# Optimization experiments

Hardware: AMD Instinct MI355X
Metric: run time of the kernel (lower is better)

Reference implementation:

```python
import jax, jax.numpy as jnp
import numpy as np
import math

INPUT_DIM = 1024
QUERY_DIM = 1024
VALUE_DIM = 1024

def setup_inputs() -> dict:
    key = jax.random.key(0)
    ks = jax.random.split(key, 7)
    N, T, D = 4, 4096, INPUT_DIM
    s_in = 1.0 / math.sqrt(D)
    X = jax.random.normal(ks[0], (N, T, D), dtype=jnp.float32)
    # torch.nn.Linear weights: (out, in), init ~ U(-1/sqrt(in), 1/sqrt(in))
    Wq = jax.random.uniform(ks[1], (QUERY_DIM, D), jnp.float32, -s_in, s_in)
    bq = jax.random.uniform(ks[2], (QUERY_DIM,), jnp.float32, -s_in, s_in)
    Wk = jax.random.uniform(ks[3], (QUERY_DIM, D), jnp.float32, -s_in, s_in)
    bk = jax.random.uniform(ks[4], (QUERY_DIM,), jnp.float32, -s_in, s_in)
    Wv = jax.random.uniform(ks[5], (VALUE_DIM, D), jnp.float32, -s_in, s_in)
    bv = jax.random.uniform(ks[6], (VALUE_DIM,), jnp.float32, -s_in, s_in)
    return {"X": X, "Wq": Wq, "bq": bq, "Wk": Wk, "bk": bk, "Wv": Wv, "bv": bv}

def reference(X, Wq, bq, Wk, bk, Wv, bv):
    N, T, D = X.shape
    q = jnp.einsum('ntd,qd->ntq', X, Wq) + bq  # (N,T,Q)
    k = jnp.einsum('ntd,qd->ntq', X, Wk) + bk  # (N,T,Q)
    v = jnp.einsum('ntd,vd->ntv', X, Wv) + bv  # (N,T,V)
    # NOTE: original scales by sqrt(D) = sqrt(input_dim), not sqrt(query_dim)
    scores = jnp.einsum('ntq,nsq->nts', q, k) / jnp.sqrt(jnp.asarray(D, X.dtype))
    attn = jax.nn.softmax(scores, axis=-1)  # (N,T,T)
    return jnp.einsum('nts,nsv->ntv', attn, v)
```

## Files before the change

kernel.cpp:

```cpp
#include <hip/hip_runtime.h>
#include <stdint.h>

typedef unsigned short u16;
typedef unsigned char u8;
typedef unsigned int u32;
typedef short shortx8 __attribute__((ext_vector_type(8)));
typedef float floatx4 __attribute__((ext_vector_type(4)));
typedef int intx4 __attribute__((ext_vector_type(4)));
typedef int intx8 __attribute__((ext_vector_type(8)));

__device__ __forceinline__ u16 f2bf(float f) {
    u32 u = __builtin_bit_cast(u32, f);
    u = (u + 0x7fffu + ((u >> 16) & 1u)) >> 16;
    return (u16)u;
}

#if defined(__has_builtin)
#  if __has_builtin(__builtin_amdgcn_cvt_pk_fp8_f32)
#    define HAVE_CVT_FP8 1
#  endif
#  if __has_builtin(__builtin_amdgcn_global_load_lds)
#    define HAVE_GLL 1
#  endif
#endif
#ifndef HAVE_CVT_FP8
#  define HAVE_CVT_FP8 0
#endif
#ifndef HAVE_GLL
#  define HAVE_GLL 0
#endif

__device__ __forceinline__ u8 f2fp8(float f) {
#if HAVE_CVT_FP8
    return (u8)(__builtin_amdgcn_cvt_pk_fp8_f32(f, f, 0, false) & 0xff);
#else
    u32 u = __builtin_bit_cast(u32, f);
    u32 s = (u >> 24) & 0x80u;
    u32 m = u & 0x7fffffffu;
    if (m >= 0x43e00000u) return (u8)(s | 0x7eu);
    if (m < 0x3c800000u) {
        int q = __float2int_rn(__builtin_bit_cast(float, m) * 512.f);
        return (u8)(s | (u32)q);
    }
    u32 r = m + 0x7ffffu + ((m >> 20) & 1u);
    u32 code = (((r >> 23) - 120u) << 3) | ((r >> 20) & 7u);
    if (code > 0x7eu) code = 0x7eu;
    return (u8)(s | code);
#endif
}

#if HAVE_GLL
__device__ __forceinline__ void gload_lds16(const void* g, void* l) {
    __builtin_amdgcn_global_load_lds(
        (const __attribute__((address_space(1))) u32*)g,
        (__attribute__((address_space(3))) u32*)l,
        16, 0, 0);
}
#endif

template <typename OutT, int MODE, int SWZ>
__global__ __launch_bounds__(256, 2) void gemm_bt(
    const u16* __restrict__ Ag, const u16* __restrict__ Bg, OutT* __restrict__ Cg,
    int lda, int ldb, int ldc, int K,
    const float* __restrict__ aux, float scale,
    long long sAz, long long sBz, long long sCz, long long sXz,
    int swz_nhalf)
{
    __shared__ u16 smem[4][128 * 32];

    int z, mb, nb;
    if constexpr (SWZ) {
        const int f = blockIdx.x, xcd = f & 7, g = f >> 3;
        z = xcd >> 1;
        mb = g & 31;
        nb = (xcd & 1) * swz_nhalf + (g >> 5);
    } else {
        z = blockIdx.z; mb = blockIdx.y; nb = blockIdx.x;
    }
    const int m0 = mb * 128, n0 = nb * 128;

    const u16* A = Ag + (long long)z * sAz;
    const u16* B = Bg + (long long)z * sBz;
    OutT* C = Cg + (long long)z * sCz;
    const float* auxp = aux ? aux + (long long)z * sXz : nullptr;

    const int tid = threadIdx.x, lane = tid & 63, wv = tid >> 6;

    const int srow = lane >> 2;
    const int schunk = (lane & 3) * 8;
    const u16* gA0 = A + (size_t)(m0 + wv * 16 + srow) * lda + schunk;
    const u16* gA1 = gA0 + (size_t)64 * lda;
    const u16* gB0 = B + (size_t)(n0 + wv * 16 + srow) * ldb + schunk;
    const u16* gB1 = gB0 + (size_t)64 * ldb;
    const int wb = wv * 512;

    const int wm = (wv & 1) * 64, wn = (wv >> 1) * 64;
    const int mi = lane & 15, kq = lane >> 4;

    floatx4 acc[4][4] = {};

    for (int k0 = 0; k0 < K; k0 += 64) {
#if HAVE_GLL
        gload_lds16(gA0,      &smem[0][wb]);
        gload_lds16(gA1,      &smem[0][2048 + wb]);
        gload_lds16(gA0 + 32, &smem[1][wb]);
        gload_lds16(gA1 + 32, &smem[1][2048 + wb]);
        gload_lds16(gB0,      &smem[2][wb]);
        gload_lds16(gB1,      &smem[2][2048 + wb]);
        gload_lds16(gB0 + 32, &smem[3][wb]);
        gload_lds16(gB1 + 32, &smem[3][2048 + wb]);
#else
        *(shortx8*)(&smem[0][wb] + lane * 8)        = *(const shortx8*)gA0;
        *(shortx8*)(&smem[0][2048 + wb] + lane * 8) = *(const shortx8*)gA1;
        *(shortx8*)(&smem[1][wb] + lane * 8)        = *(const shortx8*)(gA0 + 32);
        *(shortx8*)(&smem[1][2048 + wb] + lane * 8) = *(const shortx8*)(gA1 + 32);
        *(shortx8*)(&smem[2][wb] + lane * 8)        = *(const shortx8*)gB0;
        *(shortx8*)(&smem[2][2048 + wb] + lane * 8) = *(const shortx8*)gB1;
        *(shortx8*)(&smem[3][wb] + lane * 8)        = *(const shortx8*)(gB0 + 32);
        *(shortx8*)(&smem[3][2048 + wb] + lane * 8) = *(const shortx8*)(gB1 + 32);
#endif
        gA0 += 64; gA1 += 64; gB0 += 64; gB1 += 64;
        __syncthreads();

#pragma unroll
        for (int h = 0; h < 2; h++) {
            const u16* Ap = smem[h];
            const u16* Bp = smem[2 + h];
            shortx8 af[4], bfr[4];
#pragma unroll
            for (int i = 0; i < 4; i++)
                af[i] = *(const shortx8*)(Ap + (wm + i * 16 + mi) * 32 + kq * 8);
#pragma unroll
            for (int j = 0; j < 4; j++)
                bfr[j] = *(const shortx8*)(Bp + (wn + j * 16 + mi) * 32 + kq * 8);
#pragma unroll
            for (int i = 0; i < 4; i++)
#pragma unroll
                for (int j = 0; j < 4; j++)
                    acc[i][j] = __builtin_amdgcn_mfma_f32_16x16x32_bf16(
                        af[i], bfr[j], acc[i][j], 0, 0, 0);
        }
        __syncthreads();
    }

    float cb[4];
    if constexpr (MODE == 1) {
#pragma unroll
        for (int j = 0; j < 4; j++) cb[j] = auxp[n0 + wn + j * 16 + mi];
    }

    if constexpr (sizeof(OutT) == 2) {
        u16* ct = &smem[0][0];
#pragma unroll
        for (int i = 0; i < 4; i++) {
#pragma unroll
            for (int r = 0; r < 4; r++) {
                const int lrow = wm + i * 16 + kq * 4 + r;
                float radd = 0.f;
                if constexpr (MODE == 2) radd = auxp[m0 + lrow];
#pragma unroll
                for (int j = 0; j < 4; j++) {
                    float v = acc[i][j][r];
                    if constexpr (MODE == 1) v += cb[j];
                    if constexpr (MODE == 2) v += radd;
                    ct[lrow * 128 + wn + j * 16 + mi] = f2bf(v);
                }
            }
        }
        __syncthreads();
#pragma unroll
        for (int it = 0; it < 8; it++) {
            const int fl = (it * 256 + tid) * 8;
            const int row = fl >> 7, col = fl & 127;
            *(uint4*)(C + (size_t)(m0 + row) * ldc + n0 + col) =
                *(const uint4*)(ct + fl);
        }
    } else if constexpr (sizeof(OutT) == 1) {
        u8* ct = (u8*)&smem[0][0];
#pragma unroll
        for (int i = 0; i < 4; i++) {
#pragma unroll
            for (int r = 0; r < 4; r++) {
                const int lrow = wm + i * 16 + kq * 4 + r;
#pragma unroll
                for (int j = 0; j < 4; j++) {
                    float v = acc[i][j][r];
                    if constexpr (MODE == 1) v += cb[j];
                    ct[lrow * 128 + wn + j * 16 + mi] = f2fp8(v);
                }
            }
        }
        __syncthreads();
        u8* base = (u8*)Cg + ((size_t)mb * 16 + nb) * 16384;
#pragma unroll
        for (int it = 0; it < 4; it++) {
            const int fl = (it * 256 + tid) * 16;
            const int row = fl >> 7, c = (fl >> 4) & 7;
            *(uint4*)(base + row * 128 + ((c ^ (row & 7)) << 4)) =
                *(const uint4*)(ct + fl);
        }
    } else {
#pragma unroll
        for (int i = 0; i < 4; i++) {
#pragma unroll
            for (int r = 0; r < 4; r++) {
                const int row = m0 + wm + i * 16 + kq * 4 + r;
                float rmul = 1.f;
                if constexpr (MODE == 4) rmul = 1.0f / auxp[row];
                OutT* crow = C + (size_t)row * ldc;
#pragma unroll
                for (int j = 0; j < 4; j++) {
                    const int col = n0 + wn + j * 16 + mi;
                    crow[col] = acc[i][j][r] * rmul;
                }
            }
        }
    }
}

__global__ __launch_bounds__(512, 2) void gemm_pv256(
    const u16* __restrict__ Pg, const u16* __restrict__ Vt,
    float* __restrict__ outg, const float* __restrict__ sums, int T, int NT)
{
    __shared__ u8 smem[2][65536];

    const int f = blockIdx.x, xcd = f & 7, g = f >> 3;
    const int z = xcd >> 1;
    const int nb = (xcd & 1) * 2 + (g >> 4);
    const int mb = g & 15;
    const int m0 = mb * 256, n0 = nb * 256;

    const u8* Pz = (const u8*)(Pg + (size_t)z * T * T);
    const u8* Vz = (const u8*)(Vt + (size_t)z * T);
    const float* sumz = sums + (size_t)z * T;

    const int tid = threadIdx.x, lane = tid & 63, wv = tid >> 6;
    const int wr = wv >> 2, wc = wv & 3;
    const int mi = lane & 15, kq = lane >> 4;

    const int srow = lane >> 3;
    const int schunk = ((lane & 7) ^ srow) << 4;
    const size_t ldPb = (size_t)T * 2, ldVb = (size_t)NT * 2;
    const u8* gsrc;
    size_t grstride;
    int lds_r0;
    if (wv < 4) {
        gsrc = Pz + (size_t)(m0 + wv * 64 + srow) * ldPb + schunk;
        grstride = ldPb * 8;
        lds_r0 = wv * 8192;
    } else {
        gsrc = Vz + (size_t)(n0 + (wv - 4) * 64 + srow) * ldVb + schunk;
        grstride = ldVb * 8;
        lds_r0 = 32768 + (wv - 4) * 8192;
    }

    const int csw0 = ((0 * 4 + kq) ^ (mi & 7)) << 4;
    const int csw1 = ((1 * 4 + kq) ^ (mi & 7)) << 4;

    floatx4 acc[8][4] = {};

    auto stage = [&](int slot, int kt) {
        const u8* s0 = gsrc + (size_t)kt * 128;
        u8* l0 = &smem[slot][lds_r0];
#if HAVE_GLL
#pragma unroll
        for (int q = 0; q < 8; q++)
            gload_lds16(s0 + (size_t)q * grstride, l0 + q * 1024);
#else
#pragma unroll
        for (int q = 0; q < 8; q++)
            *(uint4*)(l0 + q * 1024 + lane * 16) =
                *(const uint4*)(s0 + (size_t)q * grstride);
#endif
    };

    stage(0, 0);
    __syncthreads();

    for (int kt = 0; kt < 64; kt++) {
        const int s = kt & 1;
        if (kt < 63) stage(s ^ 1, kt + 1);
        __builtin_amdgcn_sched_barrier(0);

        const u8* Ab = &smem[s][0];
        const u8* Bb = &smem[s][32768];

        shortx8 bfr[4][2];
#pragma unroll
        for (int nj = 0; nj < 4; nj++) {
            const u8* p = Bb + (wc * 64 + nj * 16 + mi) * 128;
            bfr[nj][0] = *(const shortx8*)(p + csw0);
            bfr[nj][1] = *(const shortx8*)(p + csw1);
        }
#pragma unroll
        for (int mh = 0; mh < 2; mh++) {
            shortx8 af[4][2];
#pragma unroll
            for (int fi = 0; fi < 4; fi++) {
                const u8* p = Ab + (wr * 128 + (mh * 4 + fi) * 16 + mi) * 128;
                af[fi][0] = *(const shortx8*)(p + csw0);
                af[fi][1] = *(const shortx8*)(p + csw1);
            }
            __builtin_amdgcn_s_setprio(1);
#pragma unroll
            for (int ks = 0; ks < 2; ks++)
#pragma unroll
                for (int fi = 0; fi < 4; fi++)
#pragma unroll
                    for (int nj = 0; nj < 4; nj++)
                        acc[mh * 4 + fi][nj] = __builtin_amdgcn_mfma_f32_16x16x32_bf16(
                            af[fi][ks], bfr[nj][ks], acc[mh * 4 + fi][nj], 0, 0, 0);
            __builtin_amdgcn_s_setprio(0);
        }
        __syncthreads();
    }

#pragma unroll
    for (int fr = 0; fr < 8; fr++) {
#pragma unroll
        for (int r = 0; r < 4; r++) {
            const int row = m0 + wr * 128 + fr * 16 + kq * 4 + r;
            const float rmul = 1.0f / sumz[row];
            float* crow = outg + ((size_t)z * T + row) * 1024 + n0 + wc * 64 + mi;
#pragma unroll
            for (int nj = 0; nj < 4; nj++)
                crow[nj * 16] = acc[fr][nj][r] * rmul;
        }
    }
}

__device__ __forceinline__ intx8 cat8(intx4 a, intx4 b) {
    return __builtin_shufflevector(a, b, 0, 1, 2, 3, 4, 5, 6, 7);
}

template <int SWZ>
__global__ __launch_bounds__(512, 2) void gemm_fp8_scores(
    const u8* __restrict__ QKt, u16* __restrict__ Pg,
    float* __restrict__ sums, float scale, int T)
{
    __shared__ u8 smem[2][32768];

    int z, mb, nb;
    if constexpr (SWZ) {
        const int f = blockIdx.x, xcd = f & 7, g = f >> 3;
        z = xcd >> 1;
        const int s = g >> 7, t = g & 127;
        mb = (s << 3) | (t & 7);
        nb = (xcd & 1) * 16 + (t >> 3);
    } else {
        z = blockIdx.z; mb = blockIdx.y; nb = blockIdx.x;
    }
    const int m0 = mb * 128, n0 = nb * 128;

    const u8* At = QKt + ((size_t)(z * 32 + mb) * 16) * 16384;
    const u8* Bt = QKt + ((size_t)(z * 32 + nb) * 16 + 8) * 16384;
    u16* P = Pg + (size_t)z * T * T;
    float* sumz = sums + (size_t)z * T;

    const int tid = threadIdx.x, lane = tid & 63, wv = tid >> 6;
    const int wm = (wv >> 1) * 32, wn = (wv & 1) * 64;
    const int mi = lane & 15, kq = lane >> 4;
    const int xm = mi & 7;
    const int off0 = ((2 * kq) ^ xm) * 16;
    const int off1 = ((2 * kq + 1) ^ xm) * 16;

    const u8* gA = At + wv * 2048 + lane * 16;
    const u8* gB = Bt + wv * 2048 + lane * 16;

    floatx4 acc[2][4] = {};

    auto stageP = [&](int b) {
#if HAVE_GLL
        gload_lds16(gA,        &smem[b][wv * 2048]);
        gload_lds16(gA + 1024, &smem[b][wv * 2048 + 1024]);
        gload_lds16(gB,        &smem[b][16384 + wv * 2048]);
        gload_lds16(gB + 1024, &smem[b][16384 + wv * 2048 + 1024]);
#else
        *(uint4*)(&smem[b][wv * 2048] + lane * 16)         = *(const uint4*)gA;
        *(uint4*)(&smem[b][wv * 2048 + 1024] + lane * 16)  = *(const uint4*)(gA + 1024);
        *(uint4*)(&smem[b][16384 + wv * 2048] + lane * 16) = *(const uint4*)gB;
        *(uint4*)(&smem[b][16384 + wv * 2048 + 1024] + lane * 16) = *(const uint4*)(gB + 1024);
#endif
        gA += 16384; gB += 16384;
    };

    stageP(0);
    __syncthreads();

    for (int kp = 0; kp < 8; kp++) {
        const int cur = kp & 1;
        if (kp < 7) stageP(cur ^ 1);
        __builtin_amdgcn_sched_barrier(0);

        const u8* Ap = &smem[cur][0];
        const u8* Bp = &smem[cur][16384];
        intx8 af[2];
#pragma unroll
        for (int i = 0; i < 2; i++) {
            const u8* p = Ap + (wm + i * 16 + mi) * 128;
            af[i] = cat8(*(const intx4*)(p + off0), *(const intx4*)(p + off1));
        }
#pragma unroll
        for (int j = 0; j < 4; j++) {
            const u8* p = Bp + (wn + j * 16 + mi) * 128;
            const intx8 bfr = cat8(*(const intx4*)(p + off0), *(const intx4*)(p + off1));
#pragma unroll
            for (int i = 0; i < 2; i++)
                acc[i][j] = __builtin_amdgcn_mfma_scale_f32_16x16x128_f8f6f4(
                    af[i], bfr, acc[i][j], 0, 0,
                    0, 0x7f7f7f7f, 0, 0x7f7f7f7f);
        }
        __syncthreads();
    }

    u16* ct = (u16*)&smem[0][0];
#pragma unroll
    for (int i = 0; i < 2; i++) {
#pragma unroll
        for (int r = 0; r < 4; r++) {
            const int lrow = wm + i * 16 + kq * 4 + r;
            float rs = 0.f;
#pragma unroll
            for (int j = 0; j < 4; j++) {
                float v = __expf(acc[i][j][r] * scale);
                rs += v;
                ct[lrow * 128 + wn + j * 16 + mi] = f2bf(v);
            }
            rs += __shfl_xor(rs, 1);
            rs += __shfl_xor(rs, 2);
            rs += __shfl_xor(rs, 4);
            rs += __shfl_xor(rs, 8);
            if (mi == 0) atomicAdd(&sumz[m0 + lrow], rs);
        }
    }
    __syncthreads();
#pragma unroll
    for (int it = 0; it < 4; it++) {
        const int fl = (it * 512 + tid) * 8;
        const int row = fl >> 7, col = fl & 127;
        *(uint4*)(P + (size_t)(m0 + row) * T + n0 + col) = *(const uint4*)(ct + fl);
    }
}

__global__ __launch_bounds__(256) void cvt_bf16(const float* __restrict__ s,
                                                u16* __restrict__ d, int n8)
{
    int i = blockIdx.x * 256 + threadIdx.x;
    if (i >= n8) return;
    const float4* sp = (const float4*)s;
    float4 a = sp[2 * i], b = sp[2 * i + 1];
    uint4 o;
    o.x = (u32)f2bf(a.x) | ((u32)f2bf(a.y) << 16);
    o.y = (u32)f2bf(a.z) | ((u32)f2bf(a.w) << 16);
    o.z = (u32)f2bf(b.x) | ((u32)f2bf(b.y) << 16);
    o.w = (u32)f2bf(b.z) | ((u32)f2bf(b.w) << 16);
    *(uint4*)(d + 8 * i) = o;
}

__global__ void concat2(const float* __restrict__ a, const float* __restrict__ b,
                        float* __restrict__ d, int n)
{
    int i = blockIdx.x * 256 + threadIdx.x;
    if (i < n) d[i] = a[i];
    else if (i < 2 * n) d[i] = b[i - n];
}

extern "C" void kernel_launch(void* const* d_in, const int* in_sizes, int n_in,
                              void* d_out, int out_size, void* d_ws, size_t ws_size,
                              hipStream_t stream)
{
    const float* X  = (const float*)d_in[0];
    const float* Wq = (const float*)d_in[1];
    const float* bq = (const float*)d_in[2];
    const float* Wk = (const float*)d_in[3];
    const float* bk = (const float*)d_in[4];
    const float* Wv = (const float*)d_in[5];
    const float* bv = (const float*)d_in[6];
    float* out = (float*)d_out;

    const int T = 4096, NT = 4 * T;
    const long long TL = T;

    char* ws = (char*)d_ws;
    size_t off = 0;
    auto alloc = [&](size_t bytes) {
        char* p = ws + off;
        off += (bytes + 255) & ~(size_t)255;
        return p;
    };
    u16*   Wqk  = (u16*)alloc((size_t)2048 * 1024 * 2);
    u16*   Wvb  = (u16*)alloc((size_t)1024 * 1024 * 2);
    float* bqk  = (float*)alloc(2048 * 4);
    u8*    QKt  = (u8*)alloc((size_t)128 * 16 * 16384);
    u16*   Vt   = (u16*)alloc((size_t)1024 * NT * 2);
    float* sums = (float*)alloc((size_t)NT * 4);
    size_t pbase = off;
    u16*   Xb   = (u16*)alloc((size_t)NT * 1024 * 2);
    u16*   P    = Xb;

    const size_t need_batched = pbase + (size_t)4 * T * T * 2;
    const bool batched = ws_size >= need_batched;

    cvt_bf16<<<dim3((NT * 1024 / 8 + 255) / 256), dim3(256), 0, stream>>>(X, Xb, NT * 1024 / 8);
    cvt_bf16<<<dim3(512), dim3(256), 0, stream>>>(Wq, Wqk, 1024 * 1024 / 8);
    cvt_bf16<<<dim3(512), dim3(256), 0, stream>>>(Wk, Wqk + 1024 * 1024, 1024 * 1024 / 8);
    cvt_bf16<<<dim3(512), dim3(256), 0, stream>>>(Wv, Wvb, 1024 * 1024 / 8);
    concat2<<<dim3(8), dim3(256), 0, stream>>>(bq, bk, bqk, 1024);
    hipMemsetAsync(sums, 0, (size_t)NT * 4, stream);

    gemm_bt<u8, 1, 0><<<dim3(16, 128, 1), dim3(256), 0, stream>>>(
        Xb, Wqk, QKt, 1024, 1024, 0, 1024, bqk, 0.f, 0, 0, 0, 0, 0);

    gemm_bt<u16, 2, 0><<<dim3(128, 8, 1), dim3(256), 0, stream>>>(
        Wvb, Xb, Vt, 1024, 1024, NT, 1024, bv, 0.f, 0, 0, 0, 0, 0);

    if (batched) {
        gemm_fp8_scores<1><<<dim3(4096), dim3(512), 0, stream>>>(
            QKt, P, sums, 0.03125f, T);
        gemm_pv256<<<dim3(256), dim3(512), 0, stream>>>(
            P, Vt, out, sums, T, NT);
    } else {
        for (int z = 0; z < 4; z++) {
            gemm_fp8_scores<0><<<dim3(32, 32, 1), dim3(512), 0, stream>>>(
                QKt + (size_t)z * 32 * 16 * 16384, P, sums + (size_t)z * T, 0.03125f, T);
            gemm_bt<float, 4, 0><<<dim3(8, 32, 1), dim3(256), 0, stream>>>(
                P, Vt + (size_t)z * T, out + (size_t)z * T * 1024,
                T, NT, 1024, T, sums + (size_t)z * T, 0.f, 0, 0, 0, 0, 0);
        }
    }
    (void)in_sizes; (void)n_in; (void)out_size;
}
```

Measured before the change: 472.8 us.

## Load A fragments directly from global into registers in fp8 scores GEMM

The A operand of the fp8 QK^T scores kernel is no longer staged through shared memory. Each lane now loads its A fragments straight from global memory into registers, prefetching one k-step ahead, while only B stays double-buffered in LDS, which halves the LDS footprint. The goal is to cut LDS traffic and shared-memory size, which may allow more occupancy. In exchange, A rows are fetched redundantly by the wave pair sharing wm, and the global loads are strided per lane.

```diff
diff --git a/kernel.cpp b/kernel.cpp
--- a/kernel.cpp
+++ b/kernel.cpp
@@ -338,7 +338,7 @@
     const u8* __restrict__ QKt, u16* __restrict__ Pg,
     float* __restrict__ sums, float scale, int T)
 {
-    __shared__ u8 smem[2][32768];
+    __shared__ u8 smem[2][16384];
 
     int z, mb, nb;
     if constexpr (SWZ) {
@@ -364,51 +364,57 @@
     const int off0 = ((2 * kq) ^ xm) * 16;
     const int off1 = ((2 * kq + 1) ^ xm) * 16;
 
-    const u8* gA = At + wv * 2048 + lane * 16;
+    const u8* gA0 = At + (wm + mi) * 128;
+    const u8* gA1 = gA0 + 2048;
+
     const u8* gB = Bt + wv * 2048 + lane * 16;
 
     floatx4 acc[2][4] = {};
 
-    auto stageP = [&](int b) {
+    auto stageB = [&](int b) {
 #if HAVE_GLL
-        gload_lds16(gA,        &smem[b][wv * 2048]);
-        gload_lds16(gA + 1024, &smem[b][wv * 2048 + 1024]);
-        gload_lds16(gB,        &smem[b][16384 + wv * 2048]);
-        gload_lds16(gB + 1024, &smem[b][16384 + wv * 2048 + 1024]);
+        gload_lds16(gB,        &smem[b][wv * 2048]);
+        gload_lds16(gB + 1024, &smem[b][wv * 2048 + 1024]);
 #else
-        *(uint4*)(&smem[b][wv * 2048] + lane * 16)         = *(const uint4*)gA;
-        *(uint4*)(&smem[b][wv * 2048 + 1024] + lane * 16)  = *(const uint4*)(gA + 1024);
-        *(uint4*)(&smem[b][16384 + wv * 2048] + lane * 16) = *(const uint4*)gB;
-        *(uint4*)(&smem[b][16384 + wv * 2048 + 1024] + lane * 16) = *(const uint4*)(gB + 1024);
-#endif
-        gA += 16384; gB += 16384;
+        *(uint4*)(&smem[b][wv * 2048] + lane * 16)        = *(const uint4*)gB;
+        *(uint4*)(&smem[b][wv * 2048 + 1024] + lane * 16) = *(const uint4*)(gB + 1024);
+#endif
+        gB += 16384;
     };
 
-    stageP(0);
+    intx4 an0, an1, an2, an3;
+    an0 = *(const intx4*)(gA0 + off0);
+    an1 = *(const intx4*)(gA0 + off1);
+    an2 = *(const intx4*)(gA1 + off0);
+    an3 = *(const intx4*)(gA1 + off1);
+    gA0 += 16384; gA1 += 16384;
+    stageB(0);
     __syncthreads();
 
+#pragma unroll
     for (int kp = 0; kp < 8; kp++) {
         const int cur = kp & 1;
-        if (kp < 7) stageP(cur ^ 1);
+        const intx8 af0 = cat8(an0, an1);
+        const intx8 af1 = cat8(an2, an3);
+        if (kp < 7) {
+            stageB(cur ^ 1);
+            an0 = *(const intx4*)(gA0 + off0);
+            an1 = *(const intx4*)(gA0 + off1);
+            an2 = *(const intx4*)(gA1 + off0);
+            an3 = *(const intx4*)(gA1 + off1);
+            gA0 += 16384; gA1 += 16384;
+        }
         __builtin_amdgcn_sched_barrier(0);
 
-        const u8* Ap = &smem[cur][0];
-        const u8* Bp = &smem[cur][16384];
-        intx8 af[2];
-#pragma unroll
-        for (int i = 0; i < 2; i++) {
-            const u8* p = Ap + (wm + i * 16 + mi) * 128;
-            af[i] = cat8(*(const intx4*)(p + off0), *(const intx4*)(p + off1));
-        }
+        const u8* Bp = &smem[cur][0];
 #pragma unroll
         for (int j = 0; j < 4; j++) {
             const u8* p = Bp + (wn + j * 16 + mi) * 128;
             const intx8 bfr = cat8(*(const intx4*)(p + off0), *(const intx4*)(p + off1));
-#pragma unroll
-            for (int i = 0; i < 2; i++)
-                acc[i][j] = __builtin_amdgcn_mfma_scale_f32_16x16x128_f8f6f4(
-                    af[i], bfr, acc[i][j], 0, 0,
-                    0, 0x7f7f7f7f, 0, 0x7f7f7f7f);
+            acc[0][j] = __builtin_amdgcn_mfma_scale_f32_16x16x128_f8f6f4(
+                af0, bfr, acc[0][j], 0, 0, 0, 0x7f7f7f7f, 0, 0x7f7f7f7f);
+            acc[1][j] = __builtin_amdgcn_mfma_scale_f32_16x16x128_f8f6f4(
+                af1, bfr, acc[1][j], 0, 0, 0, 0x7f7f7f7f, 0, 0x7f7f7f7f);
         }
         __syncthreads();
     }
```

Result: slower. 490.9 us (+3.8%).

## Enlarge FP8 score GEMM tile to 256x256 with eight-wave 2x4 layout

Applied to the files above, without the earlier changes.

The QK^T score kernel now computes 256x256 output tiles per block instead of 128x128, with each of eight waves owning a 128x64 sub-tile (8x4 MFMA accumulators). LDS double buffers grow to 64KB each, and the grid shrinks to 1024 blocks with a simpler XCD swizzle. The goal is to raise arithmetic intensity and reuse of each staged fragment, and to cut global traffic per output. It also wraps the MFMA bursts in s_setprio. In exchange it uses far more registers and 128KB of LDS, so the 2-blocks-per-CU launch bound probably cannot be met, lowering occupancy.

```diff
diff --git a/kernel.cpp b/kernel.cpp
--- a/kernel.cpp
+++ b/kernel.cpp
@@ -338,50 +338,60 @@
     const u8* __restrict__ QKt, u16* __restrict__ Pg,
     float* __restrict__ sums, float scale, int T)
 {
-    __shared__ u8 smem[2][32768];
+    __shared__ u8 smem[2][65536];
 
     int z, mb, nb;
     if constexpr (SWZ) {
         const int f = blockIdx.x, xcd = f & 7, g = f >> 3;
         z = xcd >> 1;
-        const int s = g >> 7, t = g & 127;
-        mb = (s << 3) | (t & 7);
-        nb = (xcd & 1) * 16 + (t >> 3);
+        mb = g & 15;
+        nb = (xcd & 1) * 8 + (g >> 4);
     } else {
         z = blockIdx.z; mb = blockIdx.y; nb = blockIdx.x;
     }
-    const int m0 = mb * 128, n0 = nb * 128;
-
-    const u8* At = QKt + ((size_t)(z * 32 + mb) * 16) * 16384;
-    const u8* Bt = QKt + ((size_t)(z * 32 + nb) * 16 + 8) * 16384;
+    const int m0 = mb * 256, n0 = nb * 256;
+
+    const u8* Aq0 = QKt + ((size_t)(z * 32 + 2 * mb) * 16) * 16384;
+    const u8* Aq1 = QKt + ((size_t)(z * 32 + 2 * mb + 1) * 16) * 16384;
+    const u8* Bk0 = QKt + ((size_t)(z * 32 + 2 * nb) * 16 + 8) * 16384;
+    const u8* Bk1 = QKt + ((size_t)(z * 32 + 2 * nb + 1) * 16 + 8) * 16384;
     u16* P = Pg + (size_t)z * T * T;
     float* sumz = sums + (size_t)z * T;
 
     const int tid = threadIdx.x, lane = tid & 63, wv = tid >> 6;
-    const int wm = (wv >> 1) * 32, wn = (wv & 1) * 64;
+    const int wr = wv >> 2, wc = wv & 3;
     const int mi = lane & 15, kq = lane >> 4;
     const int xm = mi & 7;
     const int off0 = ((2 * kq) ^ xm) * 16;
     const int off1 = ((2 * kq + 1) ^ xm) * 16;
 
-    const u8* gA = At + wv * 2048 + lane * 16;
-    const u8* gB = Bt + wv * 2048 + lane * 16;
-
-    floatx4 acc[2][4] = {};
+    const u8* gsrc;
+    int ldst;
+    {
+        const int w = wv & 3, th = w >> 1, rh = w & 1;
+        if (wv < 4) {
+            gsrc = (th ? Aq1 : Aq0) + rh * 8192 + lane * 16;
+            ldst = th * 16384 + rh * 8192;
+        } else {
+            gsrc = (th ? Bk1 : Bk0) + rh * 8192 + lane * 16;
+            ldst = 32768 + th * 16384 + rh * 8192;
+        }
+    }
+
+    floatx4 acc[8][4] = {};
 
     auto stageP = [&](int b) {
 #if HAVE_GLL
-        gload_lds16(gA,        &smem[b][wv * 2048]);
-        gload_lds16(gA + 1024, &smem[b][wv * 2048 + 1024]);
-        gload_lds16(gB,        &smem[b][16384 + wv * 2048]);
-        gload_lds16(gB + 1024, &smem[b][16384 + wv * 2048 + 1024]);
+#pragma unroll
+        for (int i = 0; i < 8; i++)
+            gload_lds16(gsrc + i * 1024, &smem[b][ldst + i * 1024]);
 #else
-        *(uint4*)(&smem[b][wv * 2048] + lane * 16)         = *(const uint4*)gA;
-        *(uint4*)(&smem[b][wv * 2048 + 1024] + lane * 16)  = *(const uint4*)(gA + 1024);
-        *(uint4*)(&smem[b][16384 + wv * 2048] + lane * 16) = *(const uint4*)gB;
-        *(uint4*)(&smem[b][16384 + wv * 2048 + 1024] + lane * 16) = *(const uint4*)(gB + 1024);
-#endif
-        gA += 16384; gB += 16384;
+#pragma unroll
+        for (int i = 0; i < 8; i++)
+            *(uint4*)(&smem[b][ldst + i * 1024] + lane * 16) =
+                *(const uint4*)(gsrc + i * 1024);
+#endif
+        gsrc += 16384;
     };
 
     stageP(0);
@@ -392,39 +402,47 @@
         if (kp < 7) stageP(cur ^ 1);
         __builtin_amdgcn_sched_barrier(0);
 
-        const u8* Ap = &smem[cur][0];
-        const u8* Bp = &smem[cur][16384];
-        intx8 af[2];
-#pragma unroll
-        for (int i = 0; i < 2; i++) {
-            const u8* p = Ap + (wm + i * 16 + mi) * 128;
-            af[i] = cat8(*(const intx4*)(p + off0), *(const intx4*)(p + off1));
-        }
+        const u8* Ab = &smem[cur][0] + wr * 16384;
+        const u8* Bb = &smem[cur][32768] + (wc >> 1) * 16384;
+        intx8 bfr[4];
 #pragma unroll
         for (int j = 0; j < 4; j++) {
-            const u8* p = Bp + (wn + j * 16 + mi) * 128;
-            const intx8 bfr = cat8(*(const intx4*)(p + off0), *(const intx4*)(p + off1));
-#pragma unroll
-            for (int i = 0; i < 2; i++)
-                acc[i][j] = __builtin_amdgcn_mfma_scale_f32_16x16x128_f8f6f4(
-                    af[i], bfr, acc[i][j], 0, 0,
-                    0, 0x7f7f7f7f, 0, 0x7f7f7f7f);
+            const u8* p = Bb + ((wc & 1) * 64 + j * 16 + mi) * 128;
+            bfr[j] = cat8(*(const intx4*)(p + off0), *(const intx4*)(p + off1));
+        }
+#pragma unroll
+        for (int mh = 0; mh < 2; mh++) {
+            intx8 af[4];
+#pragma unroll
+            for (int fi = 0; fi < 4; fi++) {
+                const u8* p = Ab + ((mh * 4 + fi) * 16 + mi) * 128;
+                af[fi] = cat8(*(const intx4*)(p + off0), *(const intx4*)(p + off1));
+            }
+            __builtin_amdgcn_s_setprio(1);
+#pragma unroll
+            for (int fi = 0; fi < 4; fi++)
+#pragma unroll
+                for (int j = 0; j < 4; j++)
+                    acc[mh * 4 + fi][j] = __builtin_amdgcn_mfma_scale_f32_16x16x128_f8f6f4(
+                        af[fi], bfr[j], acc[mh * 4 + fi][j], 0, 0,
+                        0, 0x7f7f7f7f, 0, 0x7f7f7f7f);
+            __builtin_amdgcn_s_setprio(0);
         }
         __syncthreads();
     }
 
     u16* ct = (u16*)&smem[0][0];
 #pragma unroll
-    for (int i = 0; i < 2; i++) {
+    for (int fr = 0; fr < 8; fr++) {
 #pragma unroll
         for (int r = 0; r < 4; r++) {
-            const int lrow = wm + i * 16 + kq * 4 + r;
+            const int lrow = wr * 128 + fr * 16 + kq * 4 + r;
             float rs = 0.f;
 #pragma unroll
             for (int j = 0; j < 4; j++) {
-                float v = __expf(acc[i][j][r] * scale);
+                float v = __expf(acc[fr][j][r] * scale);
                 rs += v;
-                ct[lrow * 128 + wn + j * 16 + mi] = f2bf(v);
+                ct[lrow * 256 + wc * 64 + j * 16 + mi] = f2bf(v);
             }
             rs += __shfl_xor(rs, 1);
             rs += __shfl_xor(rs, 2);
@@ -435,9 +453,9 @@
     }
     __syncthreads();
 #pragma unroll
-    for (int it = 0; it < 4; it++) {
+    for (int it = 0; it < 16; it++) {
         const int fl = (it * 512 + tid) * 8;
-        const int row = fl >> 7, col = fl & 127;
+        const int row = fl >> 8, col = fl & 255;
         *(uint4*)(P + (size_t)(m0 + row) * T + n0 + col) = *(const uint4*)(ct + fl);
     }
 }
@@ -515,13 +533,13 @@
         Wvb, Xb, Vt, 1024, 1024, NT, 1024, bv, 0.f, 0, 0, 0, 0, 0);
 
     if (batched) {
-        gemm_fp8_scores<1><<<dim3(4096), dim3(512), 0, stream>>>(
+        gemm_fp8_scores<1><<<dim3(1024), dim3(512), 0, stream>>>(
             QKt, P, sums, 0.03125f, T);
         gemm_pv256<<<dim3(256), dim3(512), 0, stream>>>(
             P, Vt, out, sums, T, NT);
     } else {
         for (int z = 0; z < 4; z++) {
-            gemm_fp8_scores<0><<<dim3(32, 32, 1), dim3(512), 0, stream>>>(
+            gemm_fp8_scores<0><<<dim3(16, 16, 1), dim3(512), 0, stream>>>(
                 QKt + (size_t)z * 32 * 16 * 16384, P, sums + (size_t)z * T, 0.03125f, T);
             gemm_bt<float, 4, 0><<<dim3(8, 32, 1), dim3(256), 0, stream>>>(
                 P, Vt + (size_t)z * T, out + (size_t)z * T * 1024,
```

After: 1.097 ms. +132.0%, slower.

## Double-buffer LDS tiles in bf16 GEMM to overlap loads with MFMA

Applied to the files above, without the earlier changes.

The single shared-memory tile buffer in the bt-GEMM kernel becomes two buffers. The next K-tile is issued into the alternate buffer before the MFMA work on the current tile runs, with a sched_barrier so the loads go out first. The goal is to hide global-to-LDS latency behind compute instead of stalling at a barrier every iteration. This doubles LDS per block to 32KB, which may limit occupancy. Correctness relies on the end-of-iteration barrier waiting for the async LDS loads to finish.

```diff
diff --git a/kernel.cpp b/kernel.cpp
--- a/kernel.cpp
+++ b/kernel.cpp
@@ -66,7 +66,7 @@
     long long sAz, long long sBz, long long sCz, long long sXz,
     int swz_nhalf)
 {
-    __shared__ u16 smem[4][128 * 32];
+    __shared__ u16 smem[2][4][128 * 32];
 
     int z, mb, nb;
     if constexpr (SWZ) {
@@ -99,33 +99,43 @@
 
     floatx4 acc[4][4] = {};
 
-    for (int k0 = 0; k0 < K; k0 += 64) {
+    auto stage = [&](int b) {
+        u16 (*sb)[128 * 32] = smem[b];
 #if HAVE_GLL
-        gload_lds16(gA0,      &smem[0][wb]);
-        gload_lds16(gA1,      &smem[0][2048 + wb]);
-        gload_lds16(gA0 + 32, &smem[1][wb]);
-        gload_lds16(gA1 + 32, &smem[1][2048 + wb]);
-        gload_lds16(gB0,      &smem[2][wb]);
-        gload_lds16(gB1,      &smem[2][2048 + wb]);
-        gload_lds16(gB0 + 32, &smem[3][wb]);
-        gload_lds16(gB1 + 32, &smem[3][2048 + wb]);
+        gload_lds16(gA0,      &sb[0][wb]);
+        gload_lds16(gA1,      &sb[0][2048 + wb]);
+        gload_lds16(gA0 + 32, &sb[1][wb]);
+        gload_lds16(gA1 + 32, &sb[1][2048 + wb]);
+        gload_lds16(gB0,      &sb[2][wb]);
+        gload_lds16(gB1,      &sb[2][2048 + wb]);
+        gload_lds16(gB0 + 32, &sb[3][wb]);
+        gload_lds16(gB1 + 32, &sb[3][2048 + wb]);
 #else
-        *(shortx8*)(&smem[0][wb] + lane * 8)        = *(const shortx8*)gA0;
-        *(shortx8*)(&smem[0][2048 + wb] + lane * 8) = *(const shortx8*)gA1;
-        *(shortx8*)(&smem[1][wb] + lane * 8)        = *(const shortx8*)(gA0 + 32);
-        *(shortx8*)(&smem[1][2048 + wb] + lane * 8) = *(const shortx8*)(gA1 + 32);
-        *(shortx8*)(&smem[2][wb] + lane * 8)        = *(const shortx8*)gB0;
-        *(shortx8*)(&smem[2][2048 + wb] + lane * 8) = *(const shortx8*)gB1;
-        *(shortx8*)(&smem[3][wb] + lane * 8)        = *(const shortx8*)(gB0 + 32);
-        *(shortx8*)(&smem[3][2048 + wb] + lane * 8) = *(const shortx8*)(gB1 + 32);
+        *(shortx8*)(&sb[0][wb] + lane * 8)        = *(const shortx8*)gA0;
+        *(shortx8*)(&sb[0][2048 + wb] + lane * 8) = *(const shortx8*)gA1;
+        *(shortx8*)(&sb[1][wb] + lane * 8)        = *(const shortx8*)(gA0 + 32);
+        *(shortx8*)(&sb[1][2048 + wb] + lane * 8) = *(const shortx8*)(gA1 + 32);
+        *(shortx8*)(&sb[2][wb] + lane * 8)        = *(const shortx8*)gB0;
+        *(shortx8*)(&sb[2][2048 + wb] + lane * 8) = *(const shortx8*)gB1;
+        *(shortx8*)(&sb[3][wb] + lane * 8)        = *(const shortx8*)(gB0 + 32);
+        *(shortx8*)(&sb[3][2048 + wb] + lane * 8) = *(const shortx8*)(gB1 + 32);
 #endif
         gA0 += 64; gA1 += 64; gB0 += 64; gB1 += 64;
-        __syncthreads();
+    };
+
+    stage(0);
+    __syncthreads();
+
+    const int nk = K >> 6;
+    for (int kt = 0; kt < nk; kt++) {
+        const int cur = kt & 1;
+        if (kt + 1 < nk) stage(cur ^ 1);
+        __builtin_amdgcn_sched_barrier(0);
 
 #pragma unroll
         for (int h = 0; h < 2; h++) {
-            const u16* Ap = smem[h];
-            const u16* Bp = smem[2 + h];
+            const u16* Ap = smem[cur][h];
+            const u16* Bp = smem[cur][2 + h];
             shortx8 af[4], bfr[4];
 #pragma unroll
             for (int i = 0; i < 4; i++)
@@ -150,7 +160,7 @@
     }
 
     if constexpr (sizeof(OutT) == 2) {
-        u16* ct = &smem[0][0];
+        u16* ct = &smem[0][0][0];
 #pragma unroll
         for (int i = 0; i < 4; i++) {
 #pragma unroll
@@ -176,7 +186,7 @@
                 *(const uint4*)(ct + fl);
         }
     } else if constexpr (sizeof(OutT) == 1) {
-        u8* ct = (u8*)&smem[0][0];
+        u8* ct = (u8*)&smem[0][0][0];
 #pragma unroll
         for (int i = 0; i < 4; i++) {
 #pragma unroll
```

Measured after the change: 477.2 us. About the same (+0.9%).
